# Kernel optimization log

Measured on AMD Instinct MI355X. Metric: run time of the kernel, lower is better.

The kernel has to match this reference:

```python
import jax, jax.numpy as jnp
import numpy as np

MAX_SEQ_LEN = 128
ROPE_BASE = 10000.0
D_MODEL = 2048
N_HEADS = 16
D_HEAD = D_MODEL // N_HEADS
B = 64
T = 128


def _rope_caches(d_head, max_seq_len, base=ROPE_BASE):
    thetas = 1.0 / base ** (jnp.arange(0, d_head, 2, dtype=jnp.float32) / d_head)
    freqs = jnp.arange(max_seq_len, dtype=jnp.float32)[:, None] * thetas[None, :]
    return jnp.cos(freqs), jnp.sin(freqs)


def _apply_rope(x, cos, sin):
    # x: (..., T, d_head); cos/sin: (T, d_head/2)
    x_even = x[..., 0::2]
    x_odd = x[..., 1::2]
    rot_even = x_even * cos - x_odd * sin
    rot_odd = x_even * sin + x_odd * cos
    return jnp.stack([rot_even, rot_odd], axis=-1).reshape(x.shape)


def setup_inputs() -> dict:
    key = jax.random.key(0)
    kx, kq, kk, kv, ko = jax.random.split(key, 5)
    s = 1.0 / np.sqrt(D_MODEL)
    x = jax.random.normal(kx, (B, T, D_MODEL), dtype=jnp.float32)
    W_Q = jax.random.normal(kq, (D_MODEL, D_MODEL), dtype=jnp.float32) * s
    W_K = jax.random.normal(kk, (D_MODEL, D_MODEL), dtype=jnp.float32) * s
    W_V = jax.random.normal(kv, (D_MODEL, D_MODEL), dtype=jnp.float32) * s
    W_O = jax.random.normal(ko, (D_MODEL, D_MODEL), dtype=jnp.float32) * s
    mask = jnp.tril(jnp.ones((T, T), dtype=bool))[None, None]  # (1,1,T,T) causal
    return {"x": x, "W_Q": W_Q, "W_K": W_K, "W_V": W_V, "W_O": W_O, "mask": mask}


def reference(x, W_Q, W_K, W_V, W_O, mask):
    Bsz, Tlen, D = x.shape
    cos, sin = _rope_caches(D_HEAD, MAX_SEQ_LEN)
    cos, sin = cos[:Tlen], sin[:Tlen]

    def proj(W):
        # nn.Linear: x @ W.T ; reshape to (B, H, T, d_head)
        return (x @ W.T).reshape(Bsz, Tlen, N_HEADS, D_HEAD).transpose(0, 2, 1, 3)

    Q = _apply_rope(proj(W_Q), cos, sin)
    K = _apply_rope(proj(W_K), cos, sin)
    V = proj(W_V)

    scale = jnp.float32(np.sqrt(D_HEAD))
    scores = jnp.einsum("bhqd,bhkd->bhqk", Q, K) / scale
    scores = jnp.where(mask, scores, -jnp.inf)
    weights = jax.nn.softmax(scores, axis=-1)
    attn = jnp.einsum("bhqk,bhkd->bhqd", weights, V)
    attn = attn.transpose(0, 2, 1, 3).reshape(Bsz, Tlen, D)
    return attn @ W_O.T
```

## Files before the change

### kernel.cpp

```cpp
#include <hip/hip_runtime.h>
#include <hip/hip_bf16.h>
#include <math.h>

#define D_MODEL 2048
#define N_HEADS 16
#define D_HEAD  128
#define BATCH   64
#define SEQ     128
#define BT      (BATCH*SEQ)
#define LDF     6144
#define KOFF    2048
#define VOFF    4096

typedef __bf16 bf16;
typedef __attribute__((ext_vector_type(8))) __bf16 bf16x8;
typedef __attribute__((ext_vector_type(4))) float  f32x4;

__device__ __forceinline__ f32x4 mfma16(bf16x8 a, bf16x8 b, f32x4 c) {
    return __builtin_amdgcn_mfma_f32_16x16x32_bf16(a, b, c, 0, 0, 0);
}

__device__ __forceinline__ bf16x8 cvt8_f32(const float* p) {
    f32x4 lo = *(const f32x4*)p;
    f32x4 hi = *(const f32x4*)(p + 4);
    bf16x8 r;
    r[0] = (bf16)lo[0]; r[1] = (bf16)lo[1]; r[2] = (bf16)lo[2]; r[3] = (bf16)lo[3];
    r[4] = (bf16)hi[0]; r[5] = (bf16)hi[1]; r[6] = (bf16)hi[2]; r[7] = (bf16)hi[3];
    return r;
}

__device__ __forceinline__ void gl2lds16(const bf16* g, bf16* l) {
    __builtin_amdgcn_global_load_lds(
        (const __attribute__((address_space(1))) void*)g,
        (__attribute__((address_space(3))) void*)l, 16, 0, 0);
}

__device__ __forceinline__ bf16x8 rope8(bf16x8 v, int tpos, int pair0) {
    bf16x8 r;
    for (int m = 0; m < 4; ++m) {
        int i = pair0 + m;
        float theta = __expf((float)(2 * i) * (-9.210340371976184f / 128.0f));
        float ang   = (float)tpos * theta;
        float sn, cs;
        __sincosf(ang, &sn, &cs);
        float e = (float)v[2 * m], o = (float)v[2 * m + 1];
        r[2 * m]     = (bf16)(e * cs - o * sn);
        r[2 * m + 1] = (bf16)(e * sn + o * cs);
    }
    return r;
}

__global__ __launch_bounds__(256) void cvt_kernel(const float* __restrict__ src,
                                                  bf16* __restrict__ dst, int n8)
{
    int i = blockIdx.x * 256 + threadIdx.x;
    if (i < n8) *(bf16x8*)(dst + (size_t)i * 8) = cvt8_f32(src + (size_t)i * 8);
}

__global__ __launch_bounds__(256) void cvt_w3(const float* __restrict__ w0,
                                              const float* __restrict__ w1,
                                              const float* __restrict__ w2,
                                              bf16* __restrict__ dst)
{
    int i   = blockIdx.x * 256 + threadIdx.x;
    int sel = i >> 19;
    int off = i & ((1 << 19) - 1);
    const float* s = (sel == 0) ? w0 : (sel == 1) ? w1 : w2;
    *(bf16x8*)(dst + (size_t)i * 8) = cvt8_f32(s + (size_t)off * 8);
}

template<typename OutT>
__global__ __launch_bounds__(256) void gemm128(const bf16* __restrict__ A,
                                               const bf16* __restrict__ B,
                                               OutT* __restrict__ C,
                                               int lda, int ldb, int ldc, int K)
{
    __shared__ __align__(16) bf16 As[128 * 64];
    __shared__ __align__(16) bf16 Bs[128 * 64];

    const int tid  = threadIdx.x;
    const int w    = tid >> 6;
    const int l    = tid & 63;
    const int quad = l >> 4;
    const int ln   = l & 15;
    const int wm   = w >> 1;
    const int wn   = w & 1;

    const size_t mbase = (size_t)blockIdx.y * 128;
    const size_t nbase = (size_t)blockIdx.x * 128;

    const int srow8  = tid >> 3;
    const int schunk = (tid & 7) ^ (srow8 & 7);

    const bf16* Ap = A + (mbase + srow8) * (size_t)lda + schunk * 8;
    const bf16* Bp = B + (nbase + srow8) * (size_t)ldb + schunk * 8;

    f32x4 acc[4][4];
    for (int i = 0; i < 4; ++i)
        for (int j = 0; j < 4; ++j)
            acc[i][j] = (f32x4){0.f, 0.f, 0.f, 0.f};

    const int xr = ln & 7;

    for (int k0 = 0; k0 < K; k0 += 64) {
        for (int c = 0; c < 4; ++c) {
            gl2lds16(Ap + (size_t)c * 32 * lda + k0, &As[c * 2048 + w * 512]);
            gl2lds16(Bp + (size_t)c * 32 * ldb + k0, &Bs[c * 2048 + w * 512]);
        }
        __syncthreads();

        for (int kk = 0; kk < 2; ++kk) {
            bf16x8 af[4], bfr[4];
            const int sw = ((kk * 4 + quad) ^ xr) * 8;
            for (int i = 0; i < 4; ++i)
                af[i] = *(const bf16x8*)&As[(wm * 64 + i * 16 + ln) * 64 + sw];
            for (int j = 0; j < 4; ++j)
                bfr[j] = *(const bf16x8*)&Bs[(wn * 64 + j * 16 + ln) * 64 + sw];
            for (int i = 0; i < 4; ++i)
                for (int j = 0; j < 4; ++j)
                    acc[i][j] = mfma16(af[i], bfr[j], acc[i][j]);
        }
        __syncthreads();
    }

    for (int i = 0; i < 4; ++i)
        for (int j = 0; j < 4; ++j)
            for (int r = 0; r < 4; ++r) {
                size_t row = mbase + wm * 64 + i * 16 + quad * 4 + r;
                size_t col = nbase + wn * 64 + j * 16 + ln;
                C[row * (size_t)ldc + col] = (OutT)acc[i][j][r];
            }
}

__global__ __launch_bounds__(256) void attn_kernel(bf16* __restrict__ buf)
{
    __shared__ __align__(16) bf16 KP_lds[128 * 136];
    __shared__ __align__(16) bf16 Vt_lds[128 * 136];

    const int bh = blockIdx.x;
    const int b  = bh >> 4;
    const int h  = bh & 15;
    const size_t baseQ = (size_t)b * SEQ * LDF + (size_t)h * D_HEAD;
    const size_t baseK = baseQ + KOFF;
    const size_t baseV = baseQ + VOFF;

    const int tid  = threadIdx.x;
    const int w    = tid >> 6;
    const int l    = tid & 63;
    const int quad = l >> 4;
    const int ln   = l & 15;

    {
        int k  = tid >> 1;
        int d0 = (tid & 1) * 64;
        const bf16* kp = buf + baseK + (size_t)k * LDF + d0;
        const bf16* vp = buf + baseV + (size_t)k * LDF + d0;
        for (int c = 0; c < 8; ++c) {
            bf16x8 kv = *(const bf16x8*)(kp + c * 8);
            *(bf16x8*)&KP_lds[k * 136 + d0 + c * 8] = rope8(kv, k, d0 / 2 + c * 4);
            bf16x8 vv = *(const bf16x8*)(vp + c * 8);
            for (int j = 0; j < 8; ++j)
                Vt_lds[(d0 + c * 8 + j) * 136 + k] = vv[j];
        }
    }
    __syncthreads();

    const float rscale = 0.08838834764831845f;
    const float NEG    = -1e30f;

    f32x4 acc2[2][8];
    for (int s = 0; s < 2; ++s)
        for (int nt = 0; nt < 8; ++nt) acc2[s][nt] = (f32x4){0.f, 0.f, 0.f, 0.f};

    for (int s = 0; s < 2; ++s) {
        const int q0 = w * 32 + s * 16;
        for (int kt = 0; kt < 4; ++kt) {
            bf16x8 qa = *(const bf16x8*)(buf + baseQ + (size_t)(q0 + ln) * LDF
                                           + kt * 32 + quad * 8);
            bf16x8 a = rope8(qa, q0 + ln, kt * 16 + quad * 4);
            for (int nt = 0; nt < 8; ++nt) {
                bf16x8 bb = *(const bf16x8*)&KP_lds[(nt * 16 + ln) * 136
                                                    + kt * 32 + quad * 8];
                acc2[s][nt] = mfma16(a, bb, acc2[s][nt]);
            }
        }

        float mx[4] = {NEG, NEG, NEG, NEG};
        for (int nt = 0; nt < 8; ++nt)
            for (int r = 0; r < 4; ++r) {
                int q = q0 + quad * 4 + r;
                int c = nt * 16 + ln;
                float v = acc2[s][nt][r] * rscale;
                v = (c <= q) ? v : NEG;
                acc2[s][nt][r] = v;
                mx[r] = fmaxf(mx[r], v);
            }
        for (int m = 1; m < 16; m <<= 1)
            for (int r = 0; r < 4; ++r)
                mx[r] = fmaxf(mx[r], __shfl_xor(mx[r], m));

        float sm[4] = {0.f, 0.f, 0.f, 0.f};
        for (int nt = 0; nt < 8; ++nt)
            for (int r = 0; r < 4; ++r) {
                float p = __expf(acc2[s][nt][r] - mx[r]);
                acc2[s][nt][r] = p;
                sm[r] += p;
            }
        for (int m = 1; m < 16; m <<= 1)
            for (int r = 0; r < 4; ++r)
                sm[r] += __shfl_xor(sm[r], m);

        for (int r = 0; r < 4; ++r) sm[r] = 1.0f / sm[r];
        for (int nt = 0; nt < 8; ++nt)
            for (int r = 0; r < 4; ++r)
                acc2[s][nt][r] *= sm[r];
    }

    __syncthreads();

    for (int s = 0; s < 2; ++s)
        for (int nt = 0; nt < 8; ++nt)
            for (int r = 0; r < 4; ++r) {
                int q = w * 32 + s * 16 + quad * 4 + r;
                int c = nt * 16 + ln;
                KP_lds[q * 136 + c] = (bf16)acc2[s][nt][r];
            }

    f32x4 o[2][8];
    for (int s = 0; s < 2; ++s)
        for (int nt = 0; nt < 8; ++nt) o[s][nt] = (f32x4){0.f, 0.f, 0.f, 0.f};

    for (int kt = 0; kt < 4; ++kt) {
        bf16x8 a0 = *(const bf16x8*)&KP_lds[(w * 32 +      ln) * 136 + kt * 32 + quad * 8];
        bf16x8 a1 = *(const bf16x8*)&KP_lds[(w * 32 + 16 + ln) * 136 + kt * 32 + quad * 8];
        for (int nt = 0; nt < 8; ++nt) {
            bf16x8 bb = *(const bf16x8*)&Vt_lds[(nt * 16 + ln) * 136 + kt * 32 + quad * 8];
            o[0][nt] = mfma16(a0, bb, o[0][nt]);
            o[1][nt] = mfma16(a1, bb, o[1][nt]);
        }
    }

    for (int s = 0; s < 2; ++s)
        for (int nt = 0; nt < 8; ++nt)
            for (int r = 0; r < 4; ++r) {
                int q = w * 32 + s * 16 + quad * 4 + r;
                int d = nt * 16 + ln;
                buf[baseQ + (size_t)q * LDF + d] = (bf16)o[s][nt][r];
            }
}

extern "C" void kernel_launch(void* const* d_in, const int* in_sizes, int n_in,
                              void* d_out, int out_size, void* d_ws, size_t ws_size,
                              hipStream_t stream)
{
    const float* x  = (const float*)d_in[0];
    const float* Wq = (const float*)d_in[1];
    const float* Wk = (const float*)d_in[2];
    const float* Wv = (const float*)d_in[3];
    const float* Wo = (const float*)d_in[4];
    float* out = (float*)d_out;

    bf16* QKV = (bf16*)d_ws;
    bf16* xb  = QKV + (size_t)BT * LDF;
    bf16* WB  = xb + (size_t)BT * D_MODEL;
    bf16* WoB = xb;

    const int n8x = BT * D_MODEL / 8;
    const int n8w = D_MODEL * D_MODEL / 8;

    cvt_kernel<<<(n8x + 255) / 256, 256, 0, stream>>>(x, xb, n8x);
    cvt_w3<<<(3 * n8w) / 256, 256, 0, stream>>>(Wq, Wk, Wv, WB);

    dim3 g1(LDF / 128, BT / 128);
    gemm128<bf16><<<g1, 256, 0, stream>>>(xb, WB, QKV, D_MODEL, D_MODEL, LDF, D_MODEL);

    cvt_kernel<<<(n8w + 255) / 256, 256, 0, stream>>>(Wo, WoB, n8w);

    attn_kernel<<<BATCH * N_HEADS, 256, 0, stream>>>(QKV);

    dim3 g2(D_MODEL / 128, BT / 128);
    gemm128<float><<<g2, 256, 0, stream>>>(QKV, WoB, out, LDF, D_MODEL, D_MODEL, D_MODEL);
}
```

Before: 513.8 us.

## Replace 128x128 GEMM with double-buffered 256x256 tile GEMM using 8 waves

Replaces the 128x128-tile, 4-wave GEMM with a 256x256-tile, 8-wave kernel that double-buffers LDS. Global-to-LDS loads for tile t+2 overlap MFMA compute, with manual barriers, vmcnt waits and setprio around the MFMA groups. It also swizzles the 1D block index for L2 locality and raises per-wave register reuse. The cost is 128KB of LDS and heavy register use, and with fewer, larger tiles some CUs may sit idle for the output GEMM (8x32=256 blocks).

New measurement: 471.1 us. 1.09x faster.

```diff
diff --git a/kernel.cpp b/kernel.cpp
--- a/kernel.cpp
+++ b/kernel.cpp
@@ -69,68 +69,131 @@
     *(bf16x8*)(dst + (size_t)i * 8) = cvt8_f32(s + (size_t)off * 8);
 }
 
+
+#define BAR() __builtin_amdgcn_s_barrier()
+
+#define READ_A(BSEL, mh) do {                                                 \
+    _Pragma("unroll") for (int ii = 0; ii < 4; ++ii)                          \
+    _Pragma("unroll") for (int kk = 0; kk < 2; ++kk)                          \
+        Af[ii][kk] = *(const bf16x8*)&As[BSEL][aoff[(mh)*4+ii] + ksw[kk]];    \
+    } while (0)
+
+#define READ_B(BSEL, j0) do {                                                 \
+    _Pragma("unroll") for (int jj = 0; jj < 2; ++jj)                          \
+    _Pragma("unroll") for (int kk = 0; kk < 2; ++kk)                          \
+        Bf[(j0)+jj][kk] = *(const bf16x8*)&Bs[BSEL][bof[(j0)+jj] + ksw[kk]];  \
+    } while (0)
+
+#define MQ(i0, j0) do {                                                       \
+    __builtin_amdgcn_s_setprio(1);                                            \
+    _Pragma("unroll") for (int ii = 0; ii < 4; ++ii)                          \
+    _Pragma("unroll") for (int jj = 0; jj < 2; ++jj)                          \
+    _Pragma("unroll") for (int kk = 0; kk < 2; ++kk)                          \
+        acc[(i0)+ii][(j0)+jj] =                                               \
+            mfma16(Af[ii][kk], Bf[(j0)+jj][kk], acc[(i0)+ii][(j0)+jj]);       \
+    __builtin_amdgcn_s_setprio(0);                                            \
+    } while (0)
+
+#define STAGE(BSEL, tt) do {                                                  \
+    const size_t _k = (size_t)(tt) * 64;                                      \
+    _Pragma("unroll") for (int c = 0; c < 4; ++c) {                           \
+        gl2lds16(Ag + (size_t)c * 64 * lda + _k, &As[BSEL][c*4096 + w*512]);  \
+        gl2lds16(Bg + (size_t)c * 64 * ldb + _k, &Bs[BSEL][c*4096 + w*512]);  \
+    } } while (0)
+
+#define TILE_ITER(BSEL, tt, MODE) do {                                        \
+    READ_A(BSEL, 0); READ_B(BSEL, 0); BAR(); MQ(0, 0); BAR();                 \
+    READ_B(BSEL, 2);                  BAR(); MQ(0, 2); BAR();                 \
+    READ_A(BSEL, 1);                  BAR(); MQ(4, 2);                        \
+    __builtin_amdgcn_sched_barrier(0); BAR();                                 \
+    if (MODE == 0) STAGE(BSEL, (tt) + 2);                                     \
+    BAR(); MQ(4, 0);                                                          \
+    if (MODE == 0) asm volatile("s_waitcnt vmcnt(8)" ::: "memory");           \
+    if (MODE == 1) asm volatile("s_waitcnt vmcnt(0)" ::: "memory");           \
+    BAR(); } while (0)
+
 template<typename OutT>
-__global__ __launch_bounds__(256) void gemm128(const bf16* __restrict__ A,
-                                               const bf16* __restrict__ B,
-                                               OutT* __restrict__ C,
-                                               int lda, int ldb, int ldc, int K)
-{
-    __shared__ __align__(16) bf16 As[128 * 64];
-    __shared__ __align__(16) bf16 Bs[128 * 64];
+__global__ __launch_bounds__(512, 2) void gemm256(const bf16* __restrict__ A,
+                                                  const bf16* __restrict__ B,
+                                                  OutT* __restrict__ C,
+                                                  int lda, int ldb, int ldc,
+                                                  int K, int gx)
+{
+    __shared__ __align__(16) bf16 As[2][16384];
+    __shared__ __align__(16) bf16 Bs[2][16384];
 
     const int tid  = threadIdx.x;
     const int w    = tid >> 6;
     const int l    = tid & 63;
     const int quad = l >> 4;
     const int ln   = l & 15;
-    const int wm   = w >> 1;
-    const int wn   = w & 1;
-
-    const size_t mbase = (size_t)blockIdx.y * 128;
-    const size_t nbase = (size_t)blockIdx.x * 128;
-
-    const int srow8  = tid >> 3;
-    const int schunk = (tid & 7) ^ (srow8 & 7);
-
-    const bf16* Ap = A + (mbase + srow8) * (size_t)lda + schunk * 8;
-    const bf16* Bp = B + (nbase + srow8) * (size_t)ldb + schunk * 8;
-
-    f32x4 acc[4][4];
-    for (int i = 0; i < 4; ++i)
+    const int wm   = w >> 2;
+    const int wn   = w & 3;
+
+    const int nwg = gridDim.x;
+    const int bid = blockIdx.x;
+    const int swz = (bid & 7) * (nwg >> 3) + (bid >> 3);
+    const int bx  = swz % gx;
+    const int by  = swz / gx;
+    const size_t mbase = (size_t)by * 256;
+    const size_t nbase = (size_t)bx * 256;
+
+    const int srow   = tid >> 3;
+    const int schunk = (tid & 7) ^ (srow & 7);
+    const bf16* Ag = A + (mbase + srow) * (size_t)lda + schunk * 8;
+    const bf16* Bg = B + (nbase + srow) * (size_t)ldb + schunk * 8;
+
+    const int xr = ln & 7;
+    int aoff[8], bof[4], ksw[2];
+#pragma unroll
+    for (int i = 0; i < 8; ++i) aoff[i] = (wm * 128 + i * 16 + ln) * 64;
+#pragma unroll
+    for (int j = 0; j < 4; ++j) bof[j]  = (wn * 64  + j * 16 + ln) * 64;
+#pragma unroll
+    for (int kk = 0; kk < 2; ++kk) ksw[kk] = ((kk * 4 + quad) ^ xr) * 8;
+
+    f32x4 acc[8][4];
+#pragma unroll
+    for (int i = 0; i < 8; ++i)
+#pragma unroll
+        for (int j = 0; j < 4; ++j) acc[i][j] = (f32x4){0.f, 0.f, 0.f, 0.f};
+
+    bf16x8 Af[4][2];
+    bf16x8 Bf[4][2];
+
+    STAGE(0, 0);
+    STAGE(1, 1);
+    asm volatile("s_waitcnt vmcnt(8)" ::: "memory");
+    BAR();
+
+    const int NT = K >> 6;
+    int t = 0;
+#pragma unroll 1
+    for (; t < NT - 2; t += 2) {
+        TILE_ITER(0, t, 0);
+        TILE_ITER(1, t + 1, 0);
+    }
+    TILE_ITER(0, NT - 2, 1);
+    TILE_ITER(1, NT - 1, 2);
+
+#pragma unroll
+    for (int i = 0; i < 8; ++i)
+#pragma unroll
         for (int j = 0; j < 4; ++j)
-            acc[i][j] = (f32x4){0.f, 0.f, 0.f, 0.f};
-
-    const int xr = ln & 7;
-
-    for (int k0 = 0; k0 < K; k0 += 64) {
-        for (int c = 0; c < 4; ++c) {
-            gl2lds16(Ap + (size_t)c * 32 * lda + k0, &As[c * 2048 + w * 512]);
-            gl2lds16(Bp + (size_t)c * 32 * ldb + k0, &Bs[c * 2048 + w * 512]);
-        }
-        __syncthreads();
-
-        for (int kk = 0; kk < 2; ++kk) {
-            bf16x8 af[4], bfr[4];
-            const int sw = ((kk * 4 + quad) ^ xr) * 8;
-            for (int i = 0; i < 4; ++i)
-                af[i] = *(const bf16x8*)&As[(wm * 64 + i * 16 + ln) * 64 + sw];
-            for (int j = 0; j < 4; ++j)
-                bfr[j] = *(const bf16x8*)&Bs[(wn * 64 + j * 16 + ln) * 64 + sw];
-            for (int i = 0; i < 4; ++i)
-                for (int j = 0; j < 4; ++j)
-                    acc[i][j] = mfma16(af[i], bfr[j], acc[i][j]);
-        }
-        __syncthreads();
-    }
-
-    for (int i = 0; i < 4; ++i)
-        for (int j = 0; j < 4; ++j)
-            for (int r = 0; r < 4; ++r) {
-                size_t row = mbase + wm * 64 + i * 16 + quad * 4 + r;
+#pragma unroll
+            for (int r = 0; r < 4; ++r) {
+                size_t row = mbase + wm * 128 + i * 16 + quad * 4 + r;
                 size_t col = nbase + wn * 64 + j * 16 + ln;
                 C[row * (size_t)ldc + col] = (OutT)acc[i][j][r];
             }
 }
+
+#undef BAR
+#undef READ_A
+#undef READ_B
+#undef MQ
+#undef STAGE
+#undef TILE_ITER
 
 __global__ __launch_bounds__(256) void attn_kernel(bf16* __restrict__ buf)
 {
@@ -271,13 +334,13 @@
     cvt_kernel<<<(n8x + 255) / 256, 256, 0, stream>>>(x, xb, n8x);
     cvt_w3<<<(3 * n8w) / 256, 256, 0, stream>>>(Wq, Wk, Wv, WB);
 
-    dim3 g1(LDF / 128, BT / 128);
-    gemm128<bf16><<<g1, 256, 0, stream>>>(xb, WB, QKV, D_MODEL, D_MODEL, LDF, D_MODEL);
+    gemm256<bf16><<<dim3((LDF / 256) * (BT / 256)), 512, 0, stream>>>(
+        xb, WB, QKV, D_MODEL, D_MODEL, LDF, D_MODEL, LDF / 256);
 
     cvt_kernel<<<(n8w + 255) / 256, 256, 0, stream>>>(Wo, WoB, n8w);
 
     attn_kernel<<<BATCH * N_HEADS, 256, 0, stream>>>(QKV);
 
-    dim3 g2(D_MODEL / 128, BT / 128);
-    gemm128<float><<<g2, 256, 0, stream>>>(QKV, WoB, out, LDF, D_MODEL, D_MODEL, D_MODEL);
-}
+    gemm256<float><<<dim3((D_MODEL / 256) * (BT / 256)), 512, 0, stream>>>(
+        QKV, WoB, out, LDF, D_MODEL, D_MODEL, D_MODEL, D_MODEL / 256);
+}
```
